# Kernel optimization log

Measured on AMD Instinct MI355X. Metric: run time of the kernel, lower is better.

## Reference

```python
import jax, jax.numpy as jnp
import numpy as np

HIDDEN = 1024
HEADS = 16
D_K = HIDDEN // HEADS
B, S = 2, 2048


def setup_inputs() -> dict:
    key = jax.random.key(0)
    ks = jax.random.split(key, 11)
    sc = 1.0 / np.sqrt(HIDDEN)
    inp = {
        "q": jax.random.normal(ks[0], (B, S, HIDDEN), jnp.float32),
        "k": jax.random.normal(ks[1], (B, S, HIDDEN), jnp.float32),
        "v": jax.random.normal(ks[2], (B, S, HIDDEN), jnp.float32),
        "Wq": jax.random.normal(ks[3], (HIDDEN, HIDDEN), jnp.float32) * sc,
        "bq": jnp.zeros((HIDDEN,), jnp.float32),
        "Wk": jax.random.normal(ks[4], (HIDDEN, HIDDEN), jnp.float32) * sc,
        "bk": jnp.zeros((HIDDEN,), jnp.float32),
        "Wv": jax.random.normal(ks[5], (HIDDEN, HIDDEN), jnp.float32) * sc,
        "bv": jnp.zeros((HIDDEN,), jnp.float32),
        "Wo": jax.random.normal(ks[6], (HIDDEN, HIDDEN), jnp.float32) * sc,
        "bo": jnp.zeros((HIDDEN,), jnp.float32),
    }
    return inp


def reference(q, k, v, Wq, bq, Wk, bk, Wv, bv, Wo, bo):
    bs = q.shape[0]
    # projections; torch Linear: x @ W.T + b
    def proj(x, W, b):
        y = x @ W.T + b  # [B,S,H*Dk]
        return y.reshape(bs, -1, HEADS, D_K).transpose(0, 2, 1, 3)  # [B,h,S,Dk]
    qh, kh, vh = proj(q, Wq, bq), proj(k, Wk, bk), proj(v, Wv, bv)
    scores = jnp.einsum("bhqd,bhkd->bhqk", qh, kh) / jnp.sqrt(jnp.float32(D_K))
    attn = jax.nn.softmax(scores, axis=-1)  # dropout is identity in eval mode
    x = jnp.einsum("bhqk,bhkd->bhqd", attn, vh)
    x = x.transpose(0, 2, 1, 3).reshape(bs, -1, HEADS * D_K)
    return x @ Wo.T + bo
```

## Files before the change

kernel.cpp:

```cpp
#include <hip/hip_runtime.h>
#include <stdint.h>

#define HIDDEN 1024
#define HEADS  16
#define DK     64
#define BATCH  2
#define SEQ    2048
#define MTOT   (BATCH*SEQ)
#define QSCALE 0.1803368801111204f

typedef float  f32x4   __attribute__((ext_vector_type(4)));
typedef float  f32x16  __attribute__((ext_vector_type(16)));
typedef __bf16 bf16x8  __attribute__((ext_vector_type(8)));

__device__ __forceinline__ unsigned short f2bf(float f) {
    union { float f; uint32_t u; } x;
    x.f = f;
    uint32_t r = x.u + 0x7fffu + ((x.u >> 16) & 1u);
    return (unsigned short)(r >> 16);
}

__device__ __forceinline__ bf16x8 ld_bf8(const unsigned short* p) {
    return *reinterpret_cast<const bf16x8*>(p);
}

__device__ __forceinline__ void gload16(const void* g, void* l) {
    __builtin_amdgcn_global_load_lds(
        (const __attribute__((address_space(1))) void*)g,
        (__attribute__((address_space(3))) void*)l, 16, 0, 0);
}

__device__ __forceinline__ uint32_t pkbf(float a, float b) {
    union { __bf16 h[2]; uint32_t u; } pk;
    pk.h[0] = (__bf16)a; pk.h[1] = (__bf16)b;
    return pk.u;
}

struct Cvt7 {
    const float* s[7];
    unsigned short* d[7];
    int n8[7];
};
__global__ __launch_bounds__(256) void cvt_all(Cvt7 a) {
    int id = blockIdx.y;
    int i = blockIdx.x * blockDim.x + threadIdx.x;
    if (i >= a.n8[id]) return;
    const float4* s = reinterpret_cast<const float4*>(a.s[id]) + (size_t)i * 2;
    float4 x = s[0], y = s[1];
    union { unsigned short us[8]; uint4 v; } o;
    o.us[0] = f2bf(x.x); o.us[1] = f2bf(x.y); o.us[2] = f2bf(x.z); o.us[3] = f2bf(x.w);
    o.us[4] = f2bf(y.x); o.us[5] = f2bf(y.y); o.us[6] = f2bf(y.z); o.us[7] = f2bf(y.w);
    reinterpret_cast<uint4*>(a.d[id])[i] = o.v;
}

__device__ __forceinline__ void gemm_body(const unsigned short* __restrict__ A,
                                          const unsigned short* __restrict__ W,
                                          const float* __restrict__ bias,
                                          void* __restrict__ out, int mode, float scale) {
    __shared__ __align__(16) unsigned short Alds[128 * 64];
    __shared__ __align__(16) unsigned short Blds[128 * 64];
    const int t    = threadIdx.x;
    const int lane = t & 63;
    const int wid  = t >> 6;
    const int wm   = (wid >> 1) * 64;
    const int wn   = (wid & 1) * 64;
    const int fr   = lane & 15;
    const int fg   = lane >> 4;
    const int bm   = blockIdx.y, bn = blockIdx.x;
    const int K    = HIDDEN;

    f32x4 acc[4][4];
#pragma unroll
    for (int i = 0; i < 4; i++)
#pragma unroll
        for (int j = 0; j < 4; j++) acc[i][j] = (f32x4){0.f, 0.f, 0.f, 0.f};

    const int seg_row = t >> 3;
    const int seg_col = (t & 7) * 8;

    for (int k0 = 0; k0 < K; k0 += 64) {
#pragma unroll
        for (int i = 0; i < 4; i++) {
            int row = i * 32 + seg_row;
            const unsigned short* ga = A + (size_t)(bm * 128 + row) * K + k0 + seg_col;
            const unsigned short* gb = W + (size_t)(bn * 128 + row) * K + k0 + seg_col;
            unsigned short* la = Alds + (size_t)(i * 256 + (t & ~63)) * 8;
            unsigned short* lb = Blds + (size_t)(i * 256 + (t & ~63)) * 8;
            gload16(ga, la);
            gload16(gb, lb);
        }
        __syncthreads();
#pragma unroll
        for (int kk = 0; kk < 2; kk++) {
            bf16x8 af[4], bf[4];
#pragma unroll
            for (int mt = 0; mt < 4; mt++)
                af[mt] = ld_bf8(&Alds[(wm + mt * 16 + fr) * 64 + kk * 32 + fg * 8]);
#pragma unroll
            for (int nt = 0; nt < 4; nt++)
                bf[nt] = ld_bf8(&Blds[(wn + nt * 16 + fr) * 64 + kk * 32 + fg * 8]);
#pragma unroll
            for (int mt = 0; mt < 4; mt++)
#pragma unroll
                for (int nt = 0; nt < 4; nt++)
                    acc[mt][nt] = __builtin_amdgcn_mfma_f32_16x16x32_bf16(
                        af[mt], bf[nt], acc[mt][nt], 0, 0, 0);
        }
        __syncthreads();
    }

    const int base_row = bm * 128 + wm + fg * 4;
    const int base_col = bn * 128 + wn + fr;
#pragma unroll
    for (int mt = 0; mt < 4; mt++) {
#pragma unroll
        for (int nt = 0; nt < 4; nt++) {
            int col = base_col + nt * 16;
            float bv = bias[col];
#pragma unroll
            for (int e = 0; e < 4; e++) {
                int row = base_row + mt * 16 + e;
                float val = (acc[mt][nt][e] + bv) * scale;
                if (mode == 2) {
                    ((float*)out)[(size_t)row * HIDDEN + col] = val;
                } else {
                    int b = row >> 11, s = row & (SEQ - 1);
                    int h = col >> 6, d = col & (DK - 1);
                    size_t idx;
                    if (mode == 0)
                        idx = ((size_t)(b * HEADS + h) * SEQ + s) * DK + d;
                    else
                        idx = ((size_t)(b * HEADS + h) * DK + d) * SEQ + s;
                    ((unsigned short*)out)[idx] = f2bf(val);
                }
            }
        }
    }
}

__global__ __launch_bounds__(256) void gemm_qkv(
    const unsigned short* __restrict__ qbf, const unsigned short* __restrict__ kbf,
    const unsigned short* __restrict__ vbf, const unsigned short* __restrict__ wq,
    const unsigned short* __restrict__ wk, const unsigned short* __restrict__ wv,
    const float* __restrict__ bq, const float* __restrict__ bk,
    const float* __restrict__ bv, unsigned short* __restrict__ qh,
    unsigned short* __restrict__ kh, unsigned short* __restrict__ vt) {
    int z = blockIdx.z;
    const unsigned short* A = (z == 0) ? qbf : (z == 1) ? kbf : vbf;
    const unsigned short* W = (z == 0) ? wq : (z == 1) ? wk : wv;
    const float* bias       = (z == 0) ? bq : (z == 1) ? bk : bv;
    unsigned short* out     = (z == 0) ? qh : (z == 1) ? kh : vt;
    gemm_body(A, W, bias, out, (z == 2) ? 1 : 0, (z == 0) ? QSCALE : 1.0f);
}

__global__ __launch_bounds__(256) void gemm_out(const unsigned short* __restrict__ ctx,
                                                const unsigned short* __restrict__ wo,
                                                const float* __restrict__ bo,
                                                float* __restrict__ out) {
    gemm_body(ctx, wo, bo, out, 2, 1.0f);
}

__global__ __launch_bounds__(512, 4) void attn_kernel(const unsigned short* __restrict__ qh,
                                                      const unsigned short* __restrict__ kh,
                                                      const unsigned short* __restrict__ vt,
                                                      unsigned short* __restrict__ ctx) {
    const int t = threadIdx.x, lane = t & 63, w = t >> 6;
    const int lo = lane & 31, hi = lane >> 5;
    const int qsub = w & 3, split = w >> 2;
    const int id = blockIdx.x;
    const int g  = (id & 7) * 64 + (id >> 3);
    const int by = g >> 4;
    const int bx = g & 15;
    const size_t hb = (size_t)by * (SEQ * DK);
    const int q0 = bx * 128 + qsub * 32;

    struct KV { unsigned short K[2][2][64 * 64]; unsigned short V[2][2][64 * 64]; };
    struct MG { float Lo[4][32][64]; float Lml[4][2][64]; };
    __shared__ union SMem { KV kv; MG mg; } sm;

    const unsigned short* sp[4];
    unsigned short* dpK[4];
    int sstr[4];
#pragma unroll
    for (int i = 0; i < 4; ++i) {
        int u   = w * 4 + i;
        int isV = u >> 4;
        int ssp = (u >> 3) & 1;
        int r0  = (u & 7) * 8;
        int rl  = r0 + (lane >> 3);
        int cs  = ((lane & 7) ^ ((lane >> 3) & 7)) * 8;
        if (!isV) {
            sp[i]   = kh + hb + (size_t)(ssp * 1024 + rl) * DK + cs;
            sstr[i] = 64 * DK;
            dpK[i]  = &sm.kv.K[0][ssp][r0 * 64];
        } else {
            sp[i]   = vt + hb + (size_t)rl * SEQ + ssp * 1024 + cs;
            sstr[i] = 64;
            dpK[i]  = &sm.kv.V[0][ssp][r0 * 64];
        }
    }
    const int bufoff = 2 * 64 * 64;

    bf16x8 qf[4];
#pragma unroll
    for (int tl = 0; tl < 4; ++tl)
        qf[tl] = ld_bf8(&qh[hb + (size_t)(q0 + lo) * DK + tl * 16 + hi * 8]);

    f32x16 o0, o1;
#pragma unroll
    for (int e = 0; e < 16; ++e) { o0[e] = 0.f; o1[e] = 0.f; }
    float m = -3.0e38f, l = 0.f;

#pragma unroll
    for (int i = 0; i < 4; ++i) { gload16(sp[i], dpK[i]); sp[i] += sstr[i]; }
    __syncthreads();

    const int xr = lo & 7;

    for (int it = 0; it < 16; ++it) {
        const unsigned short* Kb = &sm.kv.K[it & 1][split][0];
        const unsigned short* Vb = &sm.kv.V[it & 1][split][0];
        if (it < 15) {
#pragma unroll
            for (int i = 0; i < 4; ++i) {
                unsigned short* d = dpK[i] + ((it & 1) ? 0 : bufoff);
                gload16(sp[i], d);
                sp[i] += sstr[i];
            }
        }
        f32x16 sA, sB;
#pragma unroll
        for (int e = 0; e < 16; ++e) { sA[e] = 0.f; sB[e] = 0.f; }
        __builtin_amdgcn_s_setprio(1);
#pragma unroll
        for (int tl = 0; tl < 4; ++tl) {
            int c = 2 * tl + hi;
            bf16x8 kfA = ld_bf8(&Kb[lo * 64 + ((c ^ xr) * 8)]);
            bf16x8 kfB = ld_bf8(&Kb[(32 + lo) * 64 + ((c ^ xr) * 8)]);
            sA = __builtin_amdgcn_mfma_f32_32x32x16_bf16(kfA, qf[tl], sA, 0, 0, 0);
            sB = __builtin_amdgcn_mfma_f32_32x32x16_bf16(kfB, qf[tl], sB, 0, 0, 0);
        }
        __builtin_amdgcn_s_setprio(0);
        float pm = sA[0];
#pragma unroll
        for (int e = 1; e < 16; ++e) pm = fmaxf(pm, sA[e]);
#pragma unroll
        for (int e = 0; e < 16; ++e) pm = fmaxf(pm, sB[e]);
        pm = fmaxf(pm, __shfl_xor(pm, 32));
        if (__any(pm > m + 8.f)) {
            float mn  = fmaxf(m, pm);
            float fac = __builtin_amdgcn_exp2f(m - mn);
            m = mn;
            l *= fac;
#pragma unroll
            for (int e = 0; e < 16; ++e) { o0[e] *= fac; o1[e] *= fac; }
        }
        float sum = 0.f;
#pragma unroll
        for (int e = 0; e < 16; ++e) {
            sA[e] = __builtin_amdgcn_exp2f(sA[e] - m);
            sB[e] = __builtin_amdgcn_exp2f(sB[e] - m);
            sum += sA[e] + sB[e];
        }
        sum += __shfl_xor(sum, 32);
        l += sum;
        uint32_t pkA[8], pkB[8];
#pragma unroll
        for (int i = 0; i < 8; ++i) {
            pkA[i] = pkbf(sA[2 * i], sA[2 * i + 1]);
            pkB[i] = pkbf(sB[2 * i], sB[2 * i + 1]);
        }
        asm volatile("v_permlane32_swap_b32 %0, %1" : "+v"(pkA[0]), "+v"(pkA[2]));
        asm volatile("v_permlane32_swap_b32 %0, %1" : "+v"(pkA[1]), "+v"(pkA[3]));
        asm volatile("v_permlane32_swap_b32 %0, %1" : "+v"(pkA[4]), "+v"(pkA[6]));
        asm volatile("v_permlane32_swap_b32 %0, %1" : "+v"(pkA[5]), "+v"(pkA[7]));
        asm volatile("v_permlane32_swap_b32 %0, %1" : "+v"(pkB[0]), "+v"(pkB[2]));
        asm volatile("v_permlane32_swap_b32 %0, %1" : "+v"(pkB[1]), "+v"(pkB[3]));
        asm volatile("v_permlane32_swap_b32 %0, %1" : "+v"(pkB[4]), "+v"(pkB[6]));
        asm volatile("v_permlane32_swap_b32 %0, %1" : "+v"(pkB[5]), "+v"(pkB[7]));
        union { uint32_t u[4]; bf16x8 v; } f0, f1, f2, f3;
        f0.u[0] = pkA[0]; f0.u[1] = pkA[1]; f0.u[2] = pkA[2]; f0.u[3] = pkA[3];
        f1.u[0] = pkA[4]; f1.u[1] = pkA[5]; f1.u[2] = pkA[6]; f1.u[3] = pkA[7];
        f2.u[0] = pkB[0]; f2.u[1] = pkB[1]; f2.u[2] = pkB[2]; f2.u[3] = pkB[3];
        f3.u[0] = pkB[4]; f3.u[1] = pkB[5]; f3.u[2] = pkB[6]; f3.u[3] = pkB[7];
        bf16x8 v00 = ld_bf8(&Vb[lo * 64 + (((0 + hi) ^ xr) * 8)]);
        bf16x8 v01 = ld_bf8(&Vb[lo * 64 + (((2 + hi) ^ xr) * 8)]);
        bf16x8 v02 = ld_bf8(&Vb[lo * 64 + (((4 + hi) ^ xr) * 8)]);
        bf16x8 v03 = ld_bf8(&Vb[lo * 64 + (((6 + hi) ^ xr) * 8)]);
        bf16x8 v10 = ld_bf8(&Vb[(32 + lo) * 64 + (((0 + hi) ^ xr) * 8)]);
        bf16x8 v11 = ld_bf8(&Vb[(32 + lo) * 64 + (((2 + hi) ^ xr) * 8)]);
        bf16x8 v12 = ld_bf8(&Vb[(32 + lo) * 64 + (((4 + hi) ^ xr) * 8)]);
        bf16x8 v13 = ld_bf8(&Vb[(32 + lo) * 64 + (((6 + hi) ^ xr) * 8)]);
        __builtin_amdgcn_s_setprio(1);
        o0 = __builtin_amdgcn_mfma_f32_32x32x16_bf16(v00, f0.v, o0, 0, 0, 0);
        o0 = __builtin_amdgcn_mfma_f32_32x32x16_bf16(v01, f1.v, o0, 0, 0, 0);
        o0 = __builtin_amdgcn_mfma_f32_32x32x16_bf16(v02, f2.v, o0, 0, 0, 0);
        o0 = __builtin_amdgcn_mfma_f32_32x32x16_bf16(v03, f3.v, o0, 0, 0, 0);
        o1 = __builtin_amdgcn_mfma_f32_32x32x16_bf16(v10, f0.v, o1, 0, 0, 0);
        o1 = __builtin_amdgcn_mfma_f32_32x32x16_bf16(v11, f1.v, o1, 0, 0, 0);
        o1 = __builtin_amdgcn_mfma_f32_32x32x16_bf16(v12, f2.v, o1, 0, 0, 0);
        o1 = __builtin_amdgcn_mfma_f32_32x32x16_bf16(v13, f3.v, o1, 0, 0, 0);
        __builtin_amdgcn_s_setprio(0);
        __syncthreads();
    }

    if (split == 1) {
#pragma unroll
        for (int e = 0; e < 16; ++e) {
            sm.mg.Lo[qsub][e][lane]      = o0[e];
            sm.mg.Lo[qsub][16 + e][lane] = o1[e];
        }
        sm.mg.Lml[qsub][0][lane] = m;
        sm.mg.Lml[qsub][1][lane] = l;
    }
    __syncthreads();
    if (split == 0) {
        float m2 = sm.mg.Lml[qsub][0][lane];
        float l2 = sm.mg.Lml[qsub][1][lane];
        float M  = fmaxf(m, m2);
        float a0 = __builtin_amdgcn_exp2f(m - M);
        float a1 = __builtin_amdgcn_exp2f(m2 - M);
        float rl = __builtin_amdgcn_rcpf(a0 * l + a1 * l2);
        const int b = by >> 4, hd = by & 15;
        unsigned short* orow = ctx + ((size_t)(b * SEQ + q0 + lo)) * HIDDEN + hd * 64;
#pragma unroll
        for (int dt = 0; dt < 2; ++dt) {
#pragma unroll
            for (int gq = 0; gq < 4; ++gq) {
                union { unsigned short us[4]; uint2 v; } pk;
#pragma unroll
                for (int c = 0; c < 4; ++c) {
                    int e = gq * 4 + c;
                    float own = dt ? o1[e] : o0[e];
                    float oth = sm.mg.Lo[qsub][dt * 16 + e][lane];
                    pk.us[c] = f2bf((own * a0 + oth * a1) * rl);
                }
                *reinterpret_cast<uint2*>(orow + dt * 32 + gq * 8 + hi * 4) = pk.v;
            }
        }
    }
}

extern "C" void kernel_launch(void* const* d_in, const int* in_sizes, int n_in,
                              void* d_out, int out_size, void* d_ws, size_t ws_size,
                              hipStream_t stream) {
    const float* q  = (const float*)d_in[0];
    const float* k  = (const float*)d_in[1];
    const float* v  = (const float*)d_in[2];
    const float* Wq = (const float*)d_in[3];
    const float* bq = (const float*)d_in[4];
    const float* Wk = (const float*)d_in[5];
    const float* bk = (const float*)d_in[6];
    const float* Wv = (const float*)d_in[7];
    const float* bv = (const float*)d_in[8];
    const float* Wo = (const float*)d_in[9];
    const float* bo = (const float*)d_in[10];

    unsigned short* qbf = (unsigned short*)d_ws;
    unsigned short* kbf = qbf + (size_t)MTOT * HIDDEN;
    unsigned short* vbf = kbf + (size_t)MTOT * HIDDEN;
    unsigned short* wqb = vbf + (size_t)MTOT * HIDDEN;
    unsigned short* wkb = wqb + (size_t)HIDDEN * HIDDEN;
    unsigned short* wvb = wkb + (size_t)HIDDEN * HIDDEN;
    unsigned short* wob = wvb + (size_t)HIDDEN * HIDDEN;
    unsigned short* qh  = wob + (size_t)HIDDEN * HIDDEN;
    unsigned short* kh  = qh + (size_t)MTOT * HIDDEN;
    unsigned short* vt  = kh + (size_t)MTOT * HIDDEN;
    unsigned short* ctx = vt + (size_t)MTOT * HIDDEN;

    const int nAct8 = MTOT * HIDDEN / 8;
    const int nW8   = HIDDEN * HIDDEN / 8;

    Cvt7 ca;
    ca.s[0] = q;  ca.d[0] = qbf; ca.n8[0] = nAct8;
    ca.s[1] = k;  ca.d[1] = kbf; ca.n8[1] = nAct8;
    ca.s[2] = v;  ca.d[2] = vbf; ca.n8[2] = nAct8;
    ca.s[3] = Wq; ca.d[3] = wqb; ca.n8[3] = nW8;
    ca.s[4] = Wk; ca.d[4] = wkb; ca.n8[4] = nW8;
    ca.s[5] = Wv; ca.d[5] = wvb; ca.n8[5] = nW8;
    ca.s[6] = Wo; ca.d[6] = wob; ca.n8[6] = nW8;
    cvt_all<<<dim3(nAct8 / 256, 7), dim3(256), 0, stream>>>(ca);

    gemm_qkv<<<dim3(HIDDEN / 128, MTOT / 128, 3), dim3(256), 0, stream>>>(
        qbf, kbf, vbf, wqb, wkb, wvb, bq, bk, bv, qh, kh, vt);

    attn_kernel<<<dim3(512), dim3(512), 0, stream>>>(qh, kh, vt, ctx);

    gemm_out<<<dim3(HIDDEN / 128, MTOT / 128), dim3(256), 0, stream>>>(
        ctx, wob, bo, (float*)d_out);
}
```

Baseline: 158.0 us.

## Double-buffer GEMM LDS tiles and XOR-swizzle layout to avoid bank conflicts

The projection GEMM now stages tiles into two LDS buffers, so the global-to-LDS load of the next K-slice is issued while MFMAs run on the current one, hiding load latency. LDS columns are XOR-swizzled by row on both store and load to reduce bank conflicts on the 16-byte fragment reads. This doubles LDS use to 64KB per block, which may lower occupancy. Correctness depends on the swizzle matching between the load and read sides and on the sync placement around buffer reuse.

```diff
diff --git a/kernel.cpp b/kernel.cpp
--- a/kernel.cpp
+++ b/kernel.cpp
@@ -57,8 +57,8 @@
                                           const unsigned short* __restrict__ W,
                                           const float* __restrict__ bias,
                                           void* __restrict__ out, int mode, float scale) {
-    __shared__ __align__(16) unsigned short Alds[128 * 64];
-    __shared__ __align__(16) unsigned short Blds[128 * 64];
+    __shared__ __align__(16) unsigned short Alds[2][128 * 64];
+    __shared__ __align__(16) unsigned short Blds[2][128 * 64];
     const int t    = threadIdx.x;
     const int lane = t & 63;
     const int wid  = t >> 6;
@@ -76,29 +76,37 @@
         for (int j = 0; j < 4; j++) acc[i][j] = (f32x4){0.f, 0.f, 0.f, 0.f};
 
     const int seg_row = t >> 3;
-    const int seg_col = (t & 7) * 8;
-
-    for (int k0 = 0; k0 < K; k0 += 64) {
+    const int seg_col = ((t & 7) ^ (seg_row & 7)) * 8;
+    const int ldst    = (t & ~63) * 8;
+
+    const unsigned short* ga = A + (size_t)(bm * 128 + seg_row) * K + seg_col;
+    const unsigned short* gb = W + (size_t)(bn * 128 + seg_row) * K + seg_col;
+
+    auto stage = [&](int k0, int buf) {
 #pragma unroll
         for (int i = 0; i < 4; i++) {
-            int row = i * 32 + seg_row;
-            const unsigned short* ga = A + (size_t)(bm * 128 + row) * K + k0 + seg_col;
-            const unsigned short* gb = W + (size_t)(bn * 128 + row) * K + k0 + seg_col;
-            unsigned short* la = Alds + (size_t)(i * 256 + (t & ~63)) * 8;
-            unsigned short* lb = Blds + (size_t)(i * 256 + (t & ~63)) * 8;
-            gload16(ga, la);
-            gload16(gb, lb);
-        }
-        __syncthreads();
+            gload16(ga + (size_t)(i * 32) * K + k0, &Alds[buf][i * 2048 + ldst]);
+            gload16(gb + (size_t)(i * 32) * K + k0, &Blds[buf][i * 2048 + ldst]);
+        }
+    };
+
+    stage(0, 0);
+    __syncthreads();
+
+    for (int ks = 0; ks < K / 64; ++ks) {
+        const int cur = ks & 1;
+        if (ks < K / 64 - 1) stage((ks + 1) * 64, cur ^ 1);
 #pragma unroll
         for (int kk = 0; kk < 2; kk++) {
             bf16x8 af[4], bf[4];
 #pragma unroll
             for (int mt = 0; mt < 4; mt++)
-                af[mt] = ld_bf8(&Alds[(wm + mt * 16 + fr) * 64 + kk * 32 + fg * 8]);
+                af[mt] = ld_bf8(&Alds[cur][(wm + mt * 16 + fr) * 64 +
+                                           (((kk * 4 + fg) ^ (fr & 7)) * 8)]);
 #pragma unroll
             for (int nt = 0; nt < 4; nt++)
-                bf[nt] = ld_bf8(&Blds[(wn + nt * 16 + fr) * 64 + kk * 32 + fg * 8]);
+                bf[nt] = ld_bf8(&Blds[cur][(wn + nt * 16 + fr) * 64 +
+                                           (((kk * 4 + fg) ^ (fr & 7)) * 8)]);
 #pragma unroll
             for (int mt = 0; mt < 4; mt++)
 #pragma unroll
```

New measurement: 147.8 us. 1.07x faster.
